# Kernel optimization log

Measured on AMD Instinct MI355X. Metric: run time of the kernel, lower is better.

Reference implementation:

```python
import jax, jax.numpy as jnp
import numpy as np

B, DIM, H, W = 8, 384, 32, 32
HEADS, SCALE = 8, 4
DK = DIM // SCALE  # 96
MLP_HID = DIM * 2
N = H * W
EPS = 1e-5


def setup_inputs() -> dict:
    key = jax.random.key(0)
    ks = iter(jax.random.split(key, 40))
    def rn(shape, scale=0.05):
        return (jax.random.normal(next(ks), shape, jnp.float32) * scale)
    d = {"decoder": jax.random.normal(next(ks), (B, DIM, H, W), jnp.float32)}
    for i in (1, 2):
        d[f"wq{i}"] = rn((HEADS, DIM, DK)); d[f"bq{i}"] = rn((HEADS, DK), 1e-6)
        d[f"wk{i}"] = rn((HEADS, DIM, DK)); d[f"bk{i}"] = rn((HEADS, DK), 1e-6)
        d[f"wv{i}"] = rn((HEADS, DIM, DIM)); d[f"bv{i}"] = rn((HEADS, DIM), 1e-6)
        d[f"wp{i}"] = rn((HEADS * DIM, DIM)); d[f"bp{i}"] = rn((DIM,), 1e-6)
    d["peg_w"] = rn((DIM, 1, 3, 3), 0.3); d["peg_b"] = rn((DIM,), 1e-6)
    d["ln1_g"] = jnp.ones((DIM,)); d["ln1_b"] = jnp.zeros((DIM,))
    d["mlpln_g"] = jnp.ones((DIM,)); d["mlpln_b"] = jnp.zeros((DIM,))
    d["mlp_w1"] = rn((DIM, MLP_HID)); d["mlp_b1"] = rn((MLP_HID,), 1e-6)
    d["mlp_w2"] = rn((MLP_HID, DIM)); d["mlp_b2"] = rn((DIM,), 1e-6)
    d["ln2_g"] = jnp.ones((DIM,)); d["ln2_b"] = jnp.zeros((DIM,))
    d["a1"] = jnp.ones((1, 1, DIM)); d["a2"] = jnp.ones((1, 1, DIM)); d["a3"] = jnp.ones((1, 1, DIM))
    return d


def _ln(x, g, b):
    mu = jnp.mean(x, -1, keepdims=True)
    var = jnp.mean(jnp.square(x - mu), -1, keepdims=True)
    return (x - mu) * jax.lax.rsqrt(var + EPS) * g + b


def _mha(q, k, v, wq, bq, wk, bk, wv, bv, wp, bp):
    # per-head projections, stacked over head axis h
    qh = jnp.einsum('bnd,hde->hbne', q, wq) + bq[:, None, None, :]  # [h,B,N,dk]
    kh = jnp.einsum('bnd,hde->hbne', k, wk) + bk[:, None, None, :]
    vh = jnp.einsum('bnd,hdf->hbnf', v, wv) + bv[:, None, None, :]  # [h,B,N,dim]
    s = jax.nn.sigmoid(jnp.einsum('hbne,hbme->hbnm', qh, kh) / np.sqrt(DK))
    o = jnp.einsum('hbnm,hbmf->hbnf', s, vh)  # [h,B,N,dim]
    cat = o.transpose(1, 2, 0, 3).reshape(q.shape[0], q.shape[1], HEADS * DIM)
    return cat @ wp + bp


def _peg(x, w, b):
    Bx, Nx, C = x.shape
    img = x.reshape(Bx, H, W, C).transpose(0, 3, 1, 2)  # NCHW
    y = jax.lax.conv_general_dilated(img, w, (1, 1), 'SAME',
                                     feature_group_count=C,
                                     dimension_numbers=('NCHW', 'OIHW', 'NCHW'))
    y = y + b[None, :, None, None]
    return y.transpose(0, 2, 3, 1).reshape(Bx, Nx, C)


def reference(decoder, wq1, bq1, wk1, bk1, wv1, bv1, wp1, bp1,
              wq2, bq2, wk2, bk2, wv2, bv2, wp2, bp2,
              peg_w, peg_b, ln1_g, ln1_b, mlpln_g, mlpln_b,
              mlp_w1, mlp_b1, mlp_w2, mlp_b2, ln2_g, ln2_b, a1, a2, a3):
    x = decoder.transpose(0, 2, 3, 1).reshape(B, N, DIM)  # [B,N,C]
    x = a1 * x + _mha(x, x, x, wq1, bq1, wk1, bk1, wv1, bv1, wp1, bp1)
    x = _peg(x, peg_w, peg_b)
    x = _ln(x, ln1_g, ln1_b)
    x = a2 * x + _mha(x, x, x, wq2, bq2, wk2, bk2, wv2, bv2, wp2, bp2)
    h = _ln(x, mlpln_g, mlpln_b)
    h = jax.nn.gelu(h @ mlp_w1 + mlp_b1, approximate=False) @ mlp_w2 + mlp_b2
    x = a3 * x + h
    x = _ln(x, ln2_g, ln2_b)
    return x.reshape(B, H, W, DIM).transpose(0, 3, 1, 2)
```

## Files before the change

### kernel.cpp

```cpp
#include <hip/hip_runtime.h>
#include <math.h>

typedef unsigned short u16;
typedef unsigned int u32;
typedef short bh8 __attribute__((ext_vector_type(8)));
typedef float f4 __attribute__((ext_vector_type(4)));

__device__ __forceinline__ float bs2f(u16 s){
  union {unsigned int u; float f;} v; v.u = ((unsigned int)s)<<16; return v.f;
}
__device__ __forceinline__ u16 f2bs(float f){
  union {float f; unsigned int u;} v; v.f = f;
  unsigned int u = v.u + 0x7fffu + ((v.u>>16)&1u);
  return (u16)(u>>16);
}

__global__ void prep_all_k(
  const float* __restrict__ wq1,const float* __restrict__ wk1,const float* __restrict__ bq1,const float* __restrict__ bk1,
  const float* __restrict__ wq2,const float* __restrict__ wk2,const float* __restrict__ bq2,const float* __restrict__ bk2,
  const float* __restrict__ wp1,const float* __restrict__ wp2,
  const float* __restrict__ wv1,const float* __restrict__ wv2,
  const float* __restrict__ w1,const float* __restrict__ b1,const float* __restrict__ w2,const float* __restrict__ b2,
  u16* __restrict__ wqkT0,u16* __restrict__ wqkT1,u16* __restrict__ wpT0,u16* __restrict__ wpT1,
  u16* __restrict__ wvb0,u16* __restrict__ wvb1,
  u16* __restrict__ w1T,u16* __restrict__ w2T,
  float* __restrict__ bqkf0,float* __restrict__ bqkf1,float* __restrict__ b1f,float* __restrict__ b2f)
{
  int t = blockIdx.x*256 + threadIdx.x;
  const int S_wqk = 1536*384, S_wp = 8*384*384, S_w1 = 768*384, S_w2 = 384*768;
  if (t < 2*S_wqk){
    const float* wq = (t<S_wqk)? wq1:wq2; const float* wk = (t<S_wqk)? wk1:wk2;
    u16* o = (t<S_wqk)? wqkT0:wqkT1; int i = (t<S_wqk)? t : t-S_wqk;
    int d = i%384, cidx = i/384;
    int c2 = (cidx<768)? cidx : cidx-768;
    int h = c2/96, e = c2-h*96;
    const float* src = (cidx<768)? wq : wk;
    o[i] = f2bs(src[(h*384+d)*96 + e]);
    return;
  }
  t -= 2*S_wqk;
  if (t < 2*S_wp){
    const float* wp = (t<S_wp)? wp1:wp2; u16* o = (t<S_wp)? wpT0:wpT1;
    int i = (t<S_wp)? t: t-S_wp;
    int f = i%384; int r = i/384; int fp = r%384; int h = r/384;
    o[i] = f2bs(wp[(h*384+f)*384 + fp]);
    return;
  }
  t -= 2*S_wp;
  if (t < 2*S_wp){
    const float* wvs = (t<S_wp)? wv1:wv2; u16* o = (t<S_wp)? wvb0:wvb1;
    int i = (t<S_wp)? t: t-S_wp;
    o[i] = f2bs(wvs[i]);
    return;
  }
  t -= 2*S_wp;
  if (t < S_w1){ int d = t%384, hid = t/384; w1T[t] = f2bs(w1[d*768+hid]); return; }
  t -= S_w1;
  if (t < S_w2){ int hid = t%768, dd = t/768; w2T[t] = f2bs(w2[hid*384+dd]); return; }
  t -= S_w2;
  if (t < 1536){ bqkf0[t] = (t<768)? bq1[t] : bk1[t-768]; return; }
  t -= 1536;
  if (t < 1536){ bqkf1[t] = (t<768)? bq2[t] : bk2[t-768]; return; }
  t -= 1536;
  if (t < 768){ b1f[t] = b1[t]; return; }
  t -= 768;
  if (t < 384){ b2f[t] = b2[t]; return; }
}

__global__ void bcomb_k(const float* __restrict__ bv, const float* __restrict__ wp, float* __restrict__ out)
{
  int i = blockIdx.x*256 + threadIdx.x;
  if (i >= 3072) return;
  int h = i/384, fp = i-h*384;
  float s = 0.f;
  for (int f=0; f<384; f++) s += bv[h*384+f] * wp[(h*384+f)*384 + fp];
  out[i] = s;
}

__global__ void t0_k(const float* __restrict__ dec, float* __restrict__ xf, u16* __restrict__ xb)
{
  int b = blockIdx.z, c0 = blockIdx.y*64, n0 = blockIdx.x*64;
  __shared__ float ts[64][65];
  for (int it=threadIdx.x; it<4096; it+=256){
    int r = it>>6, cc = it&63;
    ts[r][cc] = dec[((long)(b*384 + c0+r)<<10) + n0+cc];
  }
  __syncthreads();
  for (int it=threadIdx.x; it<4096; it+=256){
    int r = it>>6, cc = it&63;
    float s = ts[cc][r];
    long o = ((long)((b<<10)+n0+r))*384 + c0+cc;
    xb[o] = f2bs(s); xf[o] = s;
  }
}

template<int EPI>
__global__ __launch_bounds__(256,2) void gemm_k(
    const u16* __restrict__ A, int lda, long sA,
    const u16* __restrict__ BT, int ldb, long sB,
    const float* __restrict__ bias,
    void* __restrict__ out0, void* __restrict__ out1,
    long sO, int K, int ldc)
{
  __shared__ __align__(16) u16 As[128*64];
  __shared__ __align__(16) u16 Bs[128*64];
  __shared__ __align__(16) u16 Cs[(EPI==2)?128*144:8];
  const int z = blockIdx.z;
  const u16* Ab = A + (long)z*sA;
  const u16* Bb = BT + (long)z*sB;
  const int m0 = blockIdx.x*128, n0 = blockIdx.y*128;
  const int tid = threadIdx.x, lane = tid&63, wv = tid>>6;
  const int wr = wv>>1, wc = wv&1;
  const int stg_r = lane>>3;
  const int stg_u = (lane&7) ^ (lane>>3);
  f4 acc[4][4];
  #pragma unroll
  for (int i=0;i<4;i++)
    #pragma unroll
    for (int j=0;j<4;j++) acc[i][j] = (f4){0.f,0.f,0.f,0.f};
  for (int k0=0;k0<K;k0+=64){
    __syncthreads();
    #pragma unroll
    for (int q=0;q<4;q++){
      int rg = (wv*4+q)*8 + stg_r;
      const u16* ga = Ab + (long)(m0+rg)*lda + k0 + stg_u*8;
      const u16* gb = Bb + (long)(n0+rg)*ldb + k0 + stg_u*8;
      __builtin_amdgcn_global_load_lds(
        (const __attribute__((address_space(1))) unsigned int*)ga,
        (__attribute__((address_space(3))) unsigned int*)(As + (wv*4+q)*512), 16, 0, 0);
      __builtin_amdgcn_global_load_lds(
        (const __attribute__((address_space(1))) unsigned int*)gb,
        (__attribute__((address_space(3))) unsigned int*)(Bs + (wv*4+q)*512), 16, 0, 0);
    }
    __syncthreads();
    #pragma unroll
    for (int ts=0;ts<2;ts++){
      const int sl = ((ts*4 + (lane>>4)) ^ (lane&7))*8;
      bh8 af[4], bfr[4];
      #pragma unroll
      for (int i=0;i<4;i++) af[i] = *(const bh8*)&As[(wr*64+i*16+(lane&15))*64 + sl];
      #pragma unroll
      for (int j=0;j<4;j++) bfr[j] = *(const bh8*)&Bs[(wc*64+j*16+(lane&15))*64 + sl];
      #pragma unroll
      for (int i=0;i<4;i++)
        #pragma unroll
        for (int j=0;j<4;j++)
          acc[i][j] = __builtin_amdgcn_mfma_f32_16x16x32_bf16(af[i], bfr[j], acc[i][j], 0,0,0);
    }
  }
  if constexpr (EPI==0){
    u16* O = (u16*)out0 + (long)z*sO;
    #pragma unroll
    for (int i=0;i<4;i++)
      #pragma unroll
      for (int j=0;j<4;j++)
        #pragma unroll
        for (int r=0;r<4;r++){
          int m = m0 + wr*64 + i*16 + ((lane>>4)<<2) + r;
          int n = n0 + wc*64 + j*16 + (lane&15);
          O[(long)m*ldc + n] = f2bs(acc[i][j][r]);
        }
  } else if constexpr (EPI==1){
    u16* Q = (u16*)out0; u16* Ko = (u16*)out1;
    #pragma unroll
    for (int j=0;j<4;j++){
      int n = n0 + wc*64 + j*16 + (lane&15);
      float bv = bias[n];
      bool isQ = n < 768; int cc = isQ ? n : n-768;
      int h = cc/96, e = cc - h*96;
      u16* dst = isQ ? Q : Ko;
      #pragma unroll
      for (int i=0;i<4;i++)
        #pragma unroll
        for (int r=0;r<4;r++){
          int m = m0 + wr*64 + i*16 + ((lane>>4)<<2) + r;
          int bb = m>>10, nn = m&1023;
          dst[((long)((bb*8+h)*1024 + nn))*96 + e] = f2bs(acc[i][j][r]+bv);
        }
    }
  } else if constexpr (EPI==2){
    __syncthreads();
    #pragma unroll
    for (int j=0;j<4;j++){
      int nl = wc*64 + j*16 + (lane&15);
      float bv = bias[n0+nl];
      #pragma unroll
      for (int i=0;i<4;i++)
        #pragma unroll
        for (int r=0;r<4;r++){
          int ml = wr*64 + i*16 + ((lane>>4)<<2) + r;
          Cs[nl*144 + ml] = f2bs(acc[i][j][r]+bv);
        }
    }
    __syncthreads();
    u16* O = (u16*)out0;
    const int bb = m0>>10, mb = m0&1023;
    #pragma unroll
    for (int p=0;p<8;p++){
      int row = p*16 + (tid>>4), mcol = (tid&15)*8;
      bh8 vv = *(const bh8*)&Cs[row*144 + mcol];
      int n = n0 + row; int h = n/384, f = n - h*384;
      *(bh8*)(O + (long)bb*3145728 + (long)f*8192 + h*1024 + mb + mcol) = vv;
    }
  } else if constexpr (EPI==3){
    u16* O = (u16*)out0;
    #pragma unroll
    for (int j=0;j<4;j++){
      int n = n0 + wc*64 + j*16 + (lane&15);
      float bv = bias[n];
      #pragma unroll
      for (int i=0;i<4;i++)
        #pragma unroll
        for (int r=0;r<4;r++){
          int m = m0 + wr*64 + i*16 + ((lane>>4)<<2) + r;
          float v = acc[i][j][r] + bv;
          v = 0.5f*v*(1.0f + erff(v*0.70710678118f));
          O[(long)m*ldc + n] = f2bs(v);
        }
    }
  } else {
    float* O = (float*)out0;
    #pragma unroll
    for (int j=0;j<4;j++){
      int n = n0 + wc*64 + j*16 + (lane&15);
      float bv = bias[n];
      #pragma unroll
      for (int i=0;i<4;i++)
        #pragma unroll
        for (int r=0;r<4;r++){
          int m = m0 + wr*64 + i*16 + ((lane>>4)<<2) + r;
          O[(long)m*ldc + n] = acc[i][j][r] + bv;
        }
    }
  }
}

__global__ __launch_bounds__(256,2) void gemm_s_k(
  const u16* __restrict__ q, const u16* __restrict__ kk_, u16* __restrict__ S2)
{
  __shared__ __align__(16) u16 smem[128*136];
  u16* As = smem;
  u16* Bs = smem + 128*56;
  const int wg = blockIdx.x;
  const int b = wg&7, idx = wg>>3;
  const int h = idx>>6, rem = idx&63;
  const int m0 = (rem>>3)*128;
  const int n0 = (rem&7)*128;
  const u16* Ab = q   + ((long)(b*8+h)<<10)*96;
  const u16* Bb = kk_ + ((long)(b*8+h)<<10)*96;
  const int tid = threadIdx.x, lane = tid&63, wv = tid>>6;
  const int wr = wv>>1, wc = wv&1;
  f4 acc[4][4];
  #pragma unroll
  for (int i=0;i<4;i++)
    #pragma unroll
    for (int j=0;j<4;j++) acc[i][j] = (f4){0.f,0.f,0.f,0.f};
  for (int k0=0;k0<96;k0+=32){
    __syncthreads();
    #pragma unroll
    for (int u=0;u<2;u++){
      int c = tid + u*256;
      int row = c>>2, col8 = (c&3)*8;
      *(bh8*)&As[row*56+col8] = *(const bh8*)(Ab + (long)(m0+row)*96 + k0 + col8);
      *(bh8*)&Bs[row*56+col8] = *(const bh8*)(Bb + (long)(n0+row)*96 + k0 + col8);
    }
    __syncthreads();
    bh8 af[4], bfr[4];
    #pragma unroll
    for (int i=0;i<4;i++) af[i] = *(const bh8*)&As[(wr*64+i*16+(lane&15))*56 + (lane>>4)*8];
    #pragma unroll
    for (int j=0;j<4;j++) bfr[j] = *(const bh8*)&Bs[(wc*64+j*16+(lane&15))*56 + (lane>>4)*8];
    #pragma unroll
    for (int i=0;i<4;i++)
      #pragma unroll
      for (int j=0;j<4;j++)
        acc[i][j] = __builtin_amdgcn_mfma_f32_16x16x32_bf16(af[i], bfr[j], acc[i][j], 0,0,0);
  }
  const float scale = 0.1020620726f;
  __syncthreads();
  #pragma unroll
  for (int j=0;j<4;j++){
    int col = wc*64 + j*16 + (lane&15);
    #pragma unroll
    for (int i=0;i<4;i++)
      #pragma unroll
      for (int r=0;r<4;r++){
        int row = wr*64 + i*16 + ((lane>>4)<<2) + r;
        float y = acc[i][j][r]*scale;
        float sg = __builtin_amdgcn_rcpf(1.0f + __expf(-y));
        smem[row*136 + col] = f2bs(sg);
      }
  }
  __syncthreads();
  u16* O = S2 + (long)b*8388608 + (long)h*1024;
  #pragma unroll
  for (int p=0;p<8;p++){
    int c = tid + p*256;
    int row = c>>4, u = c&15;
    *(bh8*)(O + (long)(m0+row)*8192 + n0 + u*8) = *(const bh8*)&smem[row*136 + u*8];
  }
}

__global__ void init_k(const float* __restrict__ xin, const float* __restrict__ av,
                       const float* __restrict__ bpv, float* __restrict__ xo)
{
  int i = blockIdx.x*256 + threadIdx.x;
  long idx = (long)i*4;
  int c = (int)(idx % 384);
  f4 x = *(const f4*)(xin + idx);
  f4 o;
  #pragma unroll
  for (int kk=0;kk<4;kk++) o[kk] = av[c+kk]*x[kk] + bpv[c+kk];
  *(f4*)(xo + idx) = o;
}

__global__ __launch_bounds__(256,2) void gemm_big_k(
  const u16* __restrict__ S2, const u16* __restrict__ Yt, float* __restrict__ xo)
{
  __shared__ __align__(16) u16 As[128*64];
  __shared__ __align__(16) u16 Bs[128*64];
  const int wg = blockIdx.x;
  const int b = wg&7, t = wg>>3;
  const int ks = t&3, nt = (t>>2)%3, mt = t/12;
  const int m0 = mt*128, n0 = nt*128, kb0 = ks*2048;
  const u16* Ab = S2 + (long)b*8388608;
  const u16* Bb = Yt + (long)b*3145728;
  const int tid = threadIdx.x, lane = tid&63, wv = tid>>6;
  const int wr = wv>>1, wc = wv&1;
  const int stg_r = lane>>3;
  const int stg_u = (lane&7) ^ (lane>>3);
  f4 acc[4][4];
  #pragma unroll
  for (int i=0;i<4;i++)
    #pragma unroll
    for (int j=0;j<4;j++) acc[i][j] = (f4){0.f,0.f,0.f,0.f};
  for (int k0=kb0; k0<kb0+2048; k0+=64){
    __syncthreads();
    #pragma unroll
    for (int q=0;q<4;q++){
      int rg = (wv*4+q)*8 + stg_r;
      const u16* ga = Ab + (((long)(m0+rg))<<13) + k0 + stg_u*8;
      const u16* gb = Bb + (((long)(n0+rg))<<13) + k0 + stg_u*8;
      __builtin_amdgcn_global_load_lds(
        (const __attribute__((address_space(1))) unsigned int*)ga,
        (__attribute__((address_space(3))) unsigned int*)(As + (wv*4+q)*512), 16, 0, 0);
      __builtin_amdgcn_global_load_lds(
        (const __attribute__((address_space(1))) unsigned int*)gb,
        (__attribute__((address_space(3))) unsigned int*)(Bs + (wv*4+q)*512), 16, 0, 0);
    }
    __syncthreads();
    #pragma unroll
    for (int ts=0;ts<2;ts++){
      const int sl = ((ts*4 + (lane>>4)) ^ (lane&7))*8;
      bh8 af[4], bfr[4];
      #pragma unroll
      for (int i=0;i<4;i++) af[i] = *(const bh8*)&As[(wr*64+i*16+(lane&15))*64 + sl];
      #pragma unroll
      for (int j=0;j<4;j++) bfr[j] = *(const bh8*)&Bs[(wc*64+j*16+(lane&15))*64 + sl];
      #pragma unroll
      for (int i=0;i<4;i++)
        #pragma unroll
        for (int j=0;j<4;j++)
          acc[i][j] = __builtin_amdgcn_mfma_f32_16x16x32_bf16(af[i], bfr[j], acc[i][j], 0,0,0);
    }
  }
  #pragma unroll
  for (int j=0;j<4;j++){
    int n = n0 + wc*64 + j*16 + (lane&15);
    #pragma unroll
    for (int i=0;i<4;i++)
      #pragma unroll
      for (int r=0;r<4;r++){
        int m = m0 + wr*64 + i*16 + ((lane>>4)<<2) + r;
        long o = ((long)((b<<10)+m))*384 + n;
        atomicAdd(&xo[o], acc[i][j][r]);
      }
  }
}

__global__ __launch_bounds__(256) void peg_ln_k(
  const float* __restrict__ xin, const float* __restrict__ pw, const float* __restrict__ pb,
  const float* __restrict__ g, const float* __restrict__ bta,
  float* __restrict__ xo, u16* __restrict__ xbo)
{
  const int row = blockIdx.x*4 + (threadIdx.x>>6);
  const int lane = threadIdx.x&63;
  const int b = row>>10, n = row&1023;
  const int i = n>>5, j = n&31;
  const float* xb_ = xin + ((long)(b<<10))*384;
  float v[6]; float s1=0.f, s2=0.f;
  #pragma unroll
  for (int kk=0;kk<6;kk++){
    int c = lane + kk*64;
    float sum = pb[c];
    #pragma unroll
    for (int di=-1; di<=1; di++){
      int ii = i+di; if (ii<0 || ii>31) continue;
      #pragma unroll
      for (int dj=-1; dj<=1; dj++){
        int jj = j+dj; if (jj<0 || jj>31) continue;
        sum += pw[c*9 + (di+1)*3 + (dj+1)] * xb_[(long)(ii*32+jj)*384 + c];
      }
    }
    v[kk] = sum; s1 += sum; s2 += sum*sum;
  }
  #pragma unroll
  for (int m=1;m<64;m<<=1){ s1 += __shfl_xor(s1,m); s2 += __shfl_xor(s2,m); }
  float mu = s1*(1.f/384.f);
  float var = s2*(1.f/384.f) - mu*mu;
  float rsq = rsqrtf(var + 1e-5f);
  long rb = (long)row*384;
  #pragma unroll
  for (int kk=0;kk<6;kk++){
    int c = lane + kk*64;
    float vv = (v[kk]-mu)*rsq*g[c] + bta[c];
    xo[rb+c] = vv; xbo[rb+c] = f2bs(vv);
  }
}

__global__ void ln_k(const float* __restrict__ x, const float* __restrict__ g,
                     const float* __restrict__ bb, u16* __restrict__ ob)
{
  long row = blockIdx.x; int l = threadIdx.x;
  const float* xr = x + row*384;
  float v[6]; float s1=0.f, s2=0.f;
  #pragma unroll
  for (int kk=0;kk<6;kk++){ int c=l+kk*64; float t=xr[c]; v[kk]=t; s1+=t; s2+=t*t; }
  #pragma unroll
  for (int m=1;m<64;m<<=1){ s1 += __shfl_xor(s1,m); s2 += __shfl_xor(s2,m); }
  float mu = s1*(1.f/384.f);
  float var = s2*(1.f/384.f) - mu*mu;
  float rsq = rsqrtf(var + 1e-5f);
  u16* orow = ob + row*384;
  #pragma unroll
  for (int kk=0;kk<6;kk++){ int c=l+kk*64; orow[c] = f2bs((v[kk]-mu)*rsq*g[c] + bb[c]); }
}

__global__ void f1_k(const float* __restrict__ xf2, const float* __restrict__ h2f,
                     const float* __restrict__ a3, const float* __restrict__ g,
                     const float* __restrict__ bb, float* __restrict__ vb)
{
  long row = blockIdx.x; int l = threadIdx.x;
  const float* xr = xf2 + row*384; const float* hr = h2f + row*384;
  float v[6]; float s1=0.f, s2=0.f;
  #pragma unroll
  for (int kk=0;kk<6;kk++){ int c=l+kk*64; float t = a3[c]*xr[c] + hr[c]; v[kk]=t; s1+=t; s2+=t*t; }
  #pragma unroll
  for (int m=1;m<64;m<<=1){ s1 += __shfl_xor(s1,m); s2 += __shfl_xor(s2,m); }
  float mu = s1*(1.f/384.f);
  float var = s2*(1.f/384.f) - mu*mu;
  float rsq = rsqrtf(var + 1e-5f);
  float* orow = vb + row*384;
  #pragma unroll
  for (int kk=0;kk<6;kk++){ int c=l+kk*64; orow[c] = (v[kk]-mu)*rsq*g[c] + bb[c]; }
}

__global__ void f2_k(const float* __restrict__ v, float* __restrict__ o)
{
  int b = blockIdx.z, c0 = blockIdx.y*64, n0 = blockIdx.x*64;
  __shared__ float tile[64][65];
  for (int it=threadIdx.x; it<4096; it+=256){
    int r = it>>6, cc = it&63;
    tile[r][cc] = v[((long)((b<<10)+n0+r))*384 + c0+cc];
  }
  __syncthreads();
  for (int it=threadIdx.x; it<4096; it+=256){
    int r = it>>6, cc = it&63;
    o[((long)(b*384 + c0+r)<<10) + n0+cc] = tile[cc][r];
  }
}

extern "C" void kernel_launch(void* const* d_in, const int* in_sizes, int n_in,
                              void* d_out, int out_size, void* d_ws, size_t ws_size,
                              hipStream_t stream)
{
  const float* dec  = (const float*)d_in[0];
  const float* wq1  = (const float*)d_in[1];  const float* bq1 = (const float*)d_in[2];
  const float* wk1  = (const float*)d_in[3];  const float* bk1 = (const float*)d_in[4];
  const float* wv1  = (const float*)d_in[5];  const float* bv1 = (const float*)d_in[6];
  const float* wp1  = (const float*)d_in[7];  const float* bp1 = (const float*)d_in[8];
  const float* wq2  = (const float*)d_in[9];  const float* bq2 = (const float*)d_in[10];
  const float* wk2  = (const float*)d_in[11]; const float* bk2 = (const float*)d_in[12];
  const float* wv2  = (const float*)d_in[13]; const float* bv2 = (const float*)d_in[14];
  const float* wp2  = (const float*)d_in[15]; const float* bp2 = (const float*)d_in[16];
  const float* pegw = (const float*)d_in[17]; const float* pegb = (const float*)d_in[18];
  const float* ln1g = (const float*)d_in[19]; const float* ln1b = (const float*)d_in[20];
  const float* mlng = (const float*)d_in[21]; const float* mlnb = (const float*)d_in[22];
  const float* w1   = (const float*)d_in[23]; const float* b1  = (const float*)d_in[24];
  const float* w2   = (const float*)d_in[25]; const float* b2  = (const float*)d_in[26];
  const float* ln2g = (const float*)d_in[27]; const float* ln2b = (const float*)d_in[28];
  const float* a1   = (const float*)d_in[29];
  const float* a2   = (const float*)d_in[30];
  const float* a3   = (const float*)d_in[31];

  char* ws = (char*)d_ws;
  const long SZ_XF  = 8192L*384*4;
  const long SZ_XB  = 8192L*384*2;
  const long SZ_QK  = 8L*8*1024*96*2;
  const long SZ_YT  = 8L*384*8192*2;
  const long SZ_S2  = 8L*1024*8192*2;
  const long SZ_WQKT= 1536L*384*2;
  const long SZ_WCT = 3072L*384*2;
  const long SZ_WPT = 8L*384*384*2;
  const long SZ_W1T = 768L*384*2;
  const long SZ_W2T = 384L*768*2;

  long off = 0;
  float* xf   = (float*)(ws+off); off += SZ_XF;
  float* xf2  = (float*)(ws+off); off += SZ_XF;
  u16*   xb   = (u16*)  (ws+off); off += SZ_XB;
  u16*   qb   = (u16*)  (ws+off); off += SZ_QK;
  u16*   kb   = (u16*)  (ws+off); off += SZ_QK;
  u16*   Yt   = (u16*)  (ws+off); off += SZ_YT;
  u16*   S2   = (u16*)  (ws+off); off += SZ_S2;
  u16*   wqkT0= (u16*)  (ws+off); off += SZ_WQKT;
  u16*   wqkT1= (u16*)  (ws+off); off += SZ_WQKT;
  u16*   wcT0 = (u16*)  (ws+off); off += SZ_WCT;
  u16*   wcT1 = (u16*)  (ws+off); off += SZ_WCT;
  u16*   w1T  = (u16*)  (ws+off); off += SZ_W1T;
  u16*   w2T  = (u16*)  (ws+off); off += SZ_W2T;
  float* bqkf0= (float*)(ws+off); off += 1536*4;
  float* bqkf1= (float*)(ws+off); off += 1536*4;
  float* bcf0 = (float*)(ws+off); off += 3072*4;
  float* bcf1 = (float*)(ws+off); off += 3072*4;
  float* b1f  = (float*)(ws+off); off += 768*4;
  float* b2f  = (float*)(ws+off); off += 384*4;
  (void)in_sizes; (void)n_in; (void)out_size; (void)ws_size;
  u16*   wpT0 = S2;
  u16*   wpT1 = S2 + SZ_WPT/2;
  u16*   wvb0 = S2 + SZ_WPT;
  u16*   wvb1 = S2 + SZ_WPT + SZ_WPT/2;
  float* xo   = (float*)qb;
  float* h2f  = (float*)kb;
  u16*   hb   = kb;
  u16*   hidb = Yt;

  prep_all_k<<<25362,256,0,stream>>>(wq1,wk1,bq1,bk1, wq2,wk2,bq2,bk2, wp1,wp2, wv1,wv2,
                                     w1,b1,w2,b2,
                                     wqkT0,wqkT1,wpT0,wpT1,wvb0,wvb1,w1T,w2T,bqkf0,bqkf1,b1f,b2f);
  bcomb_k<<<12,256,0,stream>>>(bv1, wp1, bcf0);
  bcomb_k<<<12,256,0,stream>>>(bv2, wp2, bcf1);
  gemm_k<0><<<dim3(3,3,8),256,0,stream>>>(wpT0,384,147456, wvb0,384,147456, nullptr,
                                          wcT0,nullptr, 147456, 384, 384);
  gemm_k<0><<<dim3(3,3,8),256,0,stream>>>(wpT1,384,147456, wvb1,384,147456, nullptr,
                                          wcT1,nullptr, 147456, 384, 384);
  t0_k<<<dim3(16,6,8),256,0,stream>>>(dec, xf, xb);

  gemm_k<1><<<dim3(64,12,1),256,0,stream>>>(xb,384,0, wqkT0,384,0, bqkf0, qb,kb, 0, 384, 0);
  gemm_k<2><<<dim3(64,24,1),256,0,stream>>>(xb,384,0, wcT0,384,0, bcf0, Yt,nullptr, 0, 384, 0);
  gemm_s_k<<<4096,256,0,stream>>>(qb, kb, S2);
  init_k<<<3072,256,0,stream>>>(xf, a1, bp1, xo);
  gemm_big_k<<<768,256,0,stream>>>(S2, Yt, xo);
  peg_ln_k<<<2048,256,0,stream>>>(xo, pegw, pegb, ln1g, ln1b, xf2, xb);

  gemm_k<1><<<dim3(64,12,1),256,0,stream>>>(xb,384,0, wqkT1,384,0, bqkf1, qb,kb, 0, 384, 0);
  gemm_k<2><<<dim3(64,24,1),256,0,stream>>>(xb,384,0, wcT1,384,0, bcf1, Yt,nullptr, 0, 384, 0);
  gemm_s_k<<<4096,256,0,stream>>>(qb, kb, S2);
  init_k<<<3072,256,0,stream>>>(xf2, a2, bp2, xo);
  gemm_big_k<<<768,256,0,stream>>>(S2, Yt, xo);

  ln_k<<<8192,64,0,stream>>>(xo, mlng, mlnb, hb);
  gemm_k<3><<<dim3(64,6,1),256,0,stream>>>(hb,384,0, w1T,384,0, b1f, hidb,nullptr, 0, 384, 768);
  gemm_k<4><<<dim3(64,3,1),256,0,stream>>>(hidb,768,0, w2T,768,0, b2f, h2f,nullptr, 0, 768, 384);
  f1_k<<<8192,64,0,stream>>>(xo, h2f, a3, ln2g, ln2b, xf);
  f2_k<<<dim3(16,6,8),256,0,stream>>>(xf, (float*)d_out);
}
```

Before: 527.5 us.

## Double-buffer LDS tiles in big GEMM to overlap global loads with MFMA

Gives the big S·V GEMM kernel two LDS buffers per operand. The next K-tile is prefetched with global_load_lds while MFMAs run on the current tile, and the two barriers per iteration become one. This aims to hide global-memory latency behind compute. The cost is doubled LDS per block (64KB), which could limit occupancy with the two-blocks-per-CU launch bound, and correctness relies on the async LDS loads being waited on at the barrier.

```diff
diff --git a/kernel.cpp b/kernel.cpp
--- a/kernel.cpp
+++ b/kernel.cpp
@@ -317,8 +317,8 @@
 __global__ __launch_bounds__(256,2) void gemm_big_k(
   const u16* __restrict__ S2, const u16* __restrict__ Yt, float* __restrict__ xo)
 {
-  __shared__ __align__(16) u16 As[128*64];
-  __shared__ __align__(16) u16 Bs[128*64];
+  __shared__ __align__(16) u16 As[2][128*64];
+  __shared__ __align__(16) u16 Bs[2][128*64];
   const int wg = blockIdx.x;
   const int b = wg&7, t = wg>>3;
   const int ks = t&3, nt = (t>>2)%3, mt = t/12;
@@ -334,36 +334,46 @@
   for (int i=0;i<4;i++)
     #pragma unroll
     for (int j=0;j<4;j++) acc[i][j] = (f4){0.f,0.f,0.f,0.f};
-  for (int k0=kb0; k0<kb0+2048; k0+=64){
-    __syncthreads();
-    #pragma unroll
-    for (int q=0;q<4;q++){
-      int rg = (wv*4+q)*8 + stg_r;
-      const u16* ga = Ab + (((long)(m0+rg))<<13) + k0 + stg_u*8;
-      const u16* gb = Bb + (((long)(n0+rg))<<13) + k0 + stg_u*8;
-      __builtin_amdgcn_global_load_lds(
-        (const __attribute__((address_space(1))) unsigned int*)ga,
-        (__attribute__((address_space(3))) unsigned int*)(As + (wv*4+q)*512), 16, 0, 0);
-      __builtin_amdgcn_global_load_lds(
-        (const __attribute__((address_space(1))) unsigned int*)gb,
-        (__attribute__((address_space(3))) unsigned int*)(Bs + (wv*4+q)*512), 16, 0, 0);
-    }
-    __syncthreads();
+
+  #define STAGE_BIG(BUF, K0)                                                        \
+    _Pragma("unroll")                                                               \
+    for (int q=0;q<4;q++){                                                          \
+      int rg = (wv*4+q)*8 + stg_r;                                                  \
+      const u16* ga = Ab + (((long)(m0+rg))<<13) + (K0) + stg_u*8;                  \
+      const u16* gb = Bb + (((long)(n0+rg))<<13) + (K0) + stg_u*8;                  \
+      __builtin_amdgcn_global_load_lds(                                             \
+        (const __attribute__((address_space(1))) unsigned int*)ga,                  \
+        (__attribute__((address_space(3))) unsigned int*)(&As[BUF][0] + (wv*4+q)*512), 16, 0, 0); \
+      __builtin_amdgcn_global_load_lds(                                             \
+        (const __attribute__((address_space(1))) unsigned int*)gb,                  \
+        (__attribute__((address_space(3))) unsigned int*)(&Bs[BUF][0] + (wv*4+q)*512), 16, 0, 0); \
+    }
+
+  STAGE_BIG(0, kb0);
+  __syncthreads();
+  int cur = 0;
+  for (int it=0; it<32; ++it){
+    const int k0 = kb0 + it*64;
+    if (it < 31){ STAGE_BIG(cur^1, k0+64); }
     #pragma unroll
     for (int ts=0;ts<2;ts++){
       const int sl = ((ts*4 + (lane>>4)) ^ (lane&7))*8;
       bh8 af[4], bfr[4];
       #pragma unroll
-      for (int i=0;i<4;i++) af[i] = *(const bh8*)&As[(wr*64+i*16+(lane&15))*64 + sl];
-      #pragma unroll
-      for (int j=0;j<4;j++) bfr[j] = *(const bh8*)&Bs[(wc*64+j*16+(lane&15))*64 + sl];
+      for (int i=0;i<4;i++) af[i] = *(const bh8*)&As[cur][(wr*64+i*16+(lane&15))*64 + sl];
+      #pragma unroll
+      for (int j=0;j<4;j++) bfr[j] = *(const bh8*)&Bs[cur][(wc*64+j*16+(lane&15))*64 + sl];
       #pragma unroll
       for (int i=0;i<4;i++)
         #pragma unroll
         for (int j=0;j<4;j++)
           acc[i][j] = __builtin_amdgcn_mfma_f32_16x16x32_bf16(af[i], bfr[j], acc[i][j], 0,0,0);
     }
-  }
+    __syncthreads();
+    cur ^= 1;
+  }
+  #undef STAGE_BIG
+
   #pragma unroll
   for (int j=0;j<4;j++){
     int n = n0 + wc*64 + j*16 + (lane&15);
```

Measured after the change: 558.1 us. 1.06x slower.
